# Optimization experiments

Hardware: AMD Instinct MI355X
Metric: run time of the kernel (lower is better)

## Reference

```python
import jax, jax.numpy as jnp
import numpy as np

LAMBDA_GEOMETRY = 1.0
EPS = 1e-4  # keep log() finite, mirroring valid (0,1) predictions


def setup_inputs() -> dict:
    key = jax.random.key(0)
    k1, k2, k3, k4 = jax.random.split(key, 4)
    m, H, W = 128, 128, 128
    Y_true_score = jax.random.uniform(k1, (m, 1, H, W), dtype=jnp.float32)
    Y_pred_score = jnp.clip(jax.random.uniform(k2, (m, 1, H, W), dtype=jnp.float32), EPS, 1.0 - EPS)
    Y_true_geometry = jax.random.uniform(k3, (m, 8, H, W), dtype=jnp.float32)
    Y_pred_geometry = jax.random.uniform(k4, (m, 8, H, W), dtype=jnp.float32)
    return {
        "Y_true_score": Y_true_score,
        "Y_pred_score": Y_pred_score,
        "Y_true_geometry": Y_true_geometry,
        "Y_pred_geometry": Y_pred_geometry,
    }


def reference(Y_true_score, Y_pred_score, Y_true_geometry, Y_pred_geometry):
    m = Y_true_score.shape[0]
    # --- weighted BCE score loss ---
    beta = 1.0 - jnp.sum(Y_true_score) / Y_true_score.size
    loss_pos = -beta * Y_true_score * jnp.log(Y_pred_score)
    loss_neg = -(1.0 - beta) * (1.0 - Y_true_score) * jnp.log(1.0 - Y_pred_score)
    loss_of_score = jnp.sum(loss_pos + loss_neg) / m
    # --- smoothed-L1 (Huber) geometry loss, vectorized over [m,8,H,W] ---
    l1 = jnp.abs(Y_true_geometry - Y_pred_geometry)
    huber = jnp.where(l1 < 1.0, 0.5 * l1 * l1, l1 - 0.5)
    n_c = Y_true_geometry.shape[1]  # 8
    n_pix = m * Y_true_geometry.shape[2] * Y_true_geometry.shape[3]
    loss_of_geometry = jnp.sum(huber) / n_c / n_pix * LAMBDA_GEOMETRY
    return loss_of_score + loss_of_geometry
```

## Files before the change

kernel.cpp:

```cpp
#include <hip/hip_runtime.h>


#define THREADS 256

__global__ __launch_bounds__(THREADS) void
loss_reduce(const float4* __restrict__ yts,
            const float4* __restrict__ yps,
            const float4* __restrict__ ytg,
            const float4* __restrict__ ypg,
            float4* __restrict__ partial,
            int n_s4, int n_g4) {
    const int tid = blockIdx.x * THREADS + threadIdx.x;
    const int T   = gridDim.x * THREADS;

    float s0 = 0.f, s1 = 0.f, s2 = 0.f, sg = 0.f;

    for (int i = tid; i < n_s4; i += T) {
        float4 t = yts[i];
        float4 p = yps[i];
        s0 += (t.x + t.y) + (t.z + t.w);
        s1 += t.x * __logf(p.x) + t.y * __logf(p.y)
            + t.z * __logf(p.z) + t.w * __logf(p.w);
        s2 += (1.f - t.x) * __logf(1.f - p.x) + (1.f - t.y) * __logf(1.f - p.y)
            + (1.f - t.z) * __logf(1.f - p.z) + (1.f - t.w) * __logf(1.f - p.w);
    }

    int i = tid;
    for (; i + 3 * T < n_g4; i += 4 * T) {
        float4 t0 = ytg[i];
        float4 t1 = ytg[i + T];
        float4 t2 = ytg[i + 2 * T];
        float4 t3 = ytg[i + 3 * T];
        float4 p0 = ypg[i];
        float4 p1 = ypg[i + T];
        float4 p2 = ypg[i + 2 * T];
        float4 p3 = ypg[i + 3 * T];

        #pragma unroll
        for (int k = 0; k < 4; ++k) {
            float4 t = (k == 0) ? t0 : (k == 1) ? t1 : (k == 2) ? t2 : t3;
            float4 p = (k == 0) ? p0 : (k == 1) ? p1 : (k == 2) ? p2 : p3;
            float dx = fabsf(t.x - p.x);
            float dy = fabsf(t.y - p.y);
            float dz = fabsf(t.z - p.z);
            float dw = fabsf(t.w - p.w);
            float hx = (dx < 1.f) ? 0.5f * dx * dx : dx - 0.5f;
            float hy = (dy < 1.f) ? 0.5f * dy * dy : dy - 0.5f;
            float hz = (dz < 1.f) ? 0.5f * dz * dz : dz - 0.5f;
            float hw = (dw < 1.f) ? 0.5f * dw * dw : dw - 0.5f;
            sg += (hx + hy) + (hz + hw);
        }
    }
    for (; i < n_g4; i += T) {
        float4 t = ytg[i];
        float4 p = ypg[i];
        float dx = fabsf(t.x - p.x);
        float dy = fabsf(t.y - p.y);
        float dz = fabsf(t.z - p.z);
        float dw = fabsf(t.w - p.w);
        float hx = (dx < 1.f) ? 0.5f * dx * dx : dx - 0.5f;
        float hy = (dy < 1.f) ? 0.5f * dy * dy : dy - 0.5f;
        float hz = (dz < 1.f) ? 0.5f * dz * dz : dz - 0.5f;
        float hw = (dw < 1.f) ? 0.5f * dw * dw : dw - 0.5f;
        sg += (hx + hy) + (hz + hw);
    }

    #pragma unroll
    for (int off = 32; off > 0; off >>= 1) {
        s0 += __shfl_down(s0, off);
        s1 += __shfl_down(s1, off);
        s2 += __shfl_down(s2, off);
        sg += __shfl_down(sg, off);
    }

    __shared__ float lds[4][4];
    const int wave = threadIdx.x >> 6;
    const int lane = threadIdx.x & 63;
    if (lane == 0) {
        lds[wave][0] = s0; lds[wave][1] = s1;
        lds[wave][2] = s2; lds[wave][3] = sg;
    }
    __syncthreads();
    if (threadIdx.x == 0) {
        float4 r;
        r.x = lds[0][0] + lds[1][0] + lds[2][0] + lds[3][0];
        r.y = lds[0][1] + lds[1][1] + lds[2][1] + lds[3][1];
        r.z = lds[0][2] + lds[1][2] + lds[2][2] + lds[3][2];
        r.w = lds[0][3] + lds[1][3] + lds[2][3] + lds[3][3];
        partial[blockIdx.x] = r;
    }
}

__global__ __launch_bounds__(THREADS) void
loss_finalize(const float4* __restrict__ partial, int nblocks,
              float* __restrict__ out,
              float inv_n_score, float inv_m, float inv_geo_div) {
    float s0 = 0.f, s1 = 0.f, s2 = 0.f, sg = 0.f;
    for (int i = threadIdx.x; i < nblocks; i += THREADS) {
        float4 v = partial[i];
        s0 += v.x; s1 += v.y; s2 += v.z; sg += v.w;
    }
    #pragma unroll
    for (int off = 32; off > 0; off >>= 1) {
        s0 += __shfl_down(s0, off);
        s1 += __shfl_down(s1, off);
        s2 += __shfl_down(s2, off);
        sg += __shfl_down(sg, off);
    }
    __shared__ float lds[4][4];
    const int wave = threadIdx.x >> 6;
    const int lane = threadIdx.x & 63;
    if (lane == 0) {
        lds[wave][0] = s0; lds[wave][1] = s1;
        lds[wave][2] = s2; lds[wave][3] = sg;
    }
    __syncthreads();
    if (threadIdx.x == 0) {
        const float S0 = lds[0][0] + lds[1][0] + lds[2][0] + lds[3][0];
        const float S1 = lds[0][1] + lds[1][1] + lds[2][1] + lds[3][1];
        const float S2 = lds[0][2] + lds[1][2] + lds[2][2] + lds[3][2];
        const float SG = lds[0][3] + lds[1][3] + lds[2][3] + lds[3][3];
        const float beta = 1.f - S0 * inv_n_score;
        const float loss_score = (-beta * S1 - (1.f - beta) * S2) * inv_m;
        const float loss_geo   = SG * inv_geo_div;
        out[0] = loss_score + loss_geo;
    }
}

extern "C" void kernel_launch(void* const* d_in, const int* in_sizes, int n_in,
                              void* d_out, int out_size, void* d_ws, size_t ws_size,
                              hipStream_t stream) {
    const float4* yts = (const float4*)d_in[0];
    const float4* yps = (const float4*)d_in[1];
    const float4* ytg = (const float4*)d_in[2];
    const float4* ypg = (const float4*)d_in[3];
    float* out = (float*)d_out;
    float4* partial = (float4*)d_ws;

    const int n_score = in_sizes[0];
    const int n_geo   = in_sizes[2];
    const int n_s4 = n_score / 4;
    const int n_g4 = n_geo / 4;

    int blocks = 2048;
    const size_t need = (size_t)blocks * sizeof(float4);
    if (ws_size < need) blocks = (int)(ws_size / sizeof(float4));

    const float inv_n_score = 1.f / (float)n_score;
    const float inv_m       = 1.f / 128.f;
    const float inv_geo_div = 1.f / (8.f * (float)n_score);

    loss_reduce<<<blocks, THREADS, 0, stream>>>(yts, yps, ytg, ypg, partial,
                                                n_s4, n_g4);
    loss_finalize<<<1, THREADS, 0, stream>>>(partial, blocks, out,
                                             inv_n_score, inv_m, inv_geo_div);
}
```

Baseline: 33.23 us.

## Fuse finalize into reduce kernel via last-block atomic counter; unroll geometry loop 8x

Merges the separate finalize launch into the main reduction kernel: each block publishes its partial, bumps an atomic counter, and the last block to arrive reduces all partials and writes the result. This removes the second kernel launch but adds a memset of the counter on the stream. The geometry loop is also unrolled to eight loads in flight per thread, and launch bounds gain a minimum-occupancy hint of 4, both aimed at more memory-level parallelism.

```diff
diff --git a/kernel.cpp b/kernel.cpp
--- a/kernel.cpp
+++ b/kernel.cpp
@@ -2,14 +2,30 @@
 
 
 #define THREADS 256
+#define MAXNB 2048
 
-__global__ __launch_bounds__(THREADS) void
-loss_reduce(const float4* __restrict__ yts,
-            const float4* __restrict__ yps,
-            const float4* __restrict__ ytg,
-            const float4* __restrict__ ypg,
-            float4* __restrict__ partial,
-            int n_s4, int n_g4) {
+__device__ __forceinline__ float huber4(float4 t, float4 p) {
+    float dx = fabsf(t.x - p.x);
+    float dy = fabsf(t.y - p.y);
+    float dz = fabsf(t.z - p.z);
+    float dw = fabsf(t.w - p.w);
+    float hx = (dx < 1.f) ? 0.5f * dx * dx : dx - 0.5f;
+    float hy = (dy < 1.f) ? 0.5f * dy * dy : dy - 0.5f;
+    float hz = (dz < 1.f) ? 0.5f * dz * dz : dz - 0.5f;
+    float hw = (dw < 1.f) ? 0.5f * dw * dw : dw - 0.5f;
+    return (hx + hy) + (hz + hw);
+}
+
+__global__ __launch_bounds__(THREADS, 4) void
+loss_fused(const float4* __restrict__ yts,
+           const float4* __restrict__ yps,
+           const float4* __restrict__ ytg,
+           const float4* __restrict__ ypg,
+           float4* __restrict__ partial,
+           unsigned* __restrict__ cnt,
+           float* __restrict__ out,
+           int n_s4, int n_g4,
+           float inv_n_score, float inv_m, float inv_geo_div) {
     const int tid = blockIdx.x * THREADS + threadIdx.x;
     const int T   = gridDim.x * THREADS;
 
@@ -26,43 +42,26 @@
     }
 
     int i = tid;
-    for (; i + 3 * T < n_g4; i += 4 * T) {
-        float4 t0 = ytg[i];
-        float4 t1 = ytg[i + T];
-        float4 t2 = ytg[i + 2 * T];
-        float4 t3 = ytg[i + 3 * T];
-        float4 p0 = ypg[i];
-        float4 p1 = ypg[i + T];
-        float4 p2 = ypg[i + 2 * T];
-        float4 p3 = ypg[i + 3 * T];
-
-        #pragma unroll
-        for (int k = 0; k < 4; ++k) {
-            float4 t = (k == 0) ? t0 : (k == 1) ? t1 : (k == 2) ? t2 : t3;
-            float4 p = (k == 0) ? p0 : (k == 1) ? p1 : (k == 2) ? p2 : p3;
-            float dx = fabsf(t.x - p.x);
-            float dy = fabsf(t.y - p.y);
-            float dz = fabsf(t.z - p.z);
-            float dw = fabsf(t.w - p.w);
-            float hx = (dx < 1.f) ? 0.5f * dx * dx : dx - 0.5f;
-            float hy = (dy < 1.f) ? 0.5f * dy * dy : dy - 0.5f;
-            float hz = (dz < 1.f) ? 0.5f * dz * dz : dz - 0.5f;
-            float hw = (dw < 1.f) ? 0.5f * dw * dw : dw - 0.5f;
-            sg += (hx + hy) + (hz + hw);
-        }
+    for (; i + 7 * T < n_g4; i += 8 * T) {
+        float4 t0 = ytg[i];         float4 p0 = ypg[i];
+        float4 t1 = ytg[i + T];     float4 p1 = ypg[i + T];
+        float4 t2 = ytg[i + 2 * T]; float4 p2 = ypg[i + 2 * T];
+        float4 t3 = ytg[i + 3 * T]; float4 p3 = ypg[i + 3 * T];
+        float4 t4 = ytg[i + 4 * T]; float4 p4 = ypg[i + 4 * T];
+        float4 t5 = ytg[i + 5 * T]; float4 p5 = ypg[i + 5 * T];
+        float4 t6 = ytg[i + 6 * T]; float4 p6 = ypg[i + 6 * T];
+        float4 t7 = ytg[i + 7 * T]; float4 p7 = ypg[i + 7 * T];
+        sg += huber4(t0, p0);
+        sg += huber4(t1, p1);
+        sg += huber4(t2, p2);
+        sg += huber4(t3, p3);
+        sg += huber4(t4, p4);
+        sg += huber4(t5, p5);
+        sg += huber4(t6, p6);
+        sg += huber4(t7, p7);
     }
     for (; i < n_g4; i += T) {
-        float4 t = ytg[i];
-        float4 p = ypg[i];
-        float dx = fabsf(t.x - p.x);
-        float dy = fabsf(t.y - p.y);
-        float dz = fabsf(t.z - p.z);
-        float dw = fabsf(t.w - p.w);
-        float hx = (dx < 1.f) ? 0.5f * dx * dx : dx - 0.5f;
-        float hy = (dy < 1.f) ? 0.5f * dy * dy : dy - 0.5f;
-        float hz = (dz < 1.f) ? 0.5f * dz * dz : dz - 0.5f;
-        float hw = (dw < 1.f) ? 0.5f * dw * dw : dw - 0.5f;
-        sg += (hx + hy) + (hz + hw);
+        sg += huber4(ytg[i], ypg[i]);
     }
 
     #pragma unroll
@@ -74,6 +73,7 @@
     }
 
     __shared__ float lds[4][4];
+    __shared__ int is_last;
     const int wave = threadIdx.x >> 6;
     const int lane = threadIdx.x & 63;
     if (lane == 0) {
@@ -88,42 +88,42 @@
         r.z = lds[0][2] + lds[1][2] + lds[2][2] + lds[3][2];
         r.w = lds[0][3] + lds[1][3] + lds[2][3] + lds[3][3];
         partial[blockIdx.x] = r;
-    }
-}
-
-__global__ __launch_bounds__(THREADS) void
-loss_finalize(const float4* __restrict__ partial, int nblocks,
-              float* __restrict__ out,
-              float inv_n_score, float inv_m, float inv_geo_div) {
-    float s0 = 0.f, s1 = 0.f, s2 = 0.f, sg = 0.f;
-    for (int i = threadIdx.x; i < nblocks; i += THREADS) {
-        float4 v = partial[i];
-        s0 += v.x; s1 += v.y; s2 += v.z; sg += v.w;
-    }
-    #pragma unroll
-    for (int off = 32; off > 0; off >>= 1) {
-        s0 += __shfl_down(s0, off);
-        s1 += __shfl_down(s1, off);
-        s2 += __shfl_down(s2, off);
-        sg += __shfl_down(sg, off);
-    }
-    __shared__ float lds[4][4];
-    const int wave = threadIdx.x >> 6;
-    const int lane = threadIdx.x & 63;
-    if (lane == 0) {
-        lds[wave][0] = s0; lds[wave][1] = s1;
-        lds[wave][2] = s2; lds[wave][3] = sg;
+        __threadfence();
+        unsigned old = atomicAdd(cnt, 1u);
+        is_last = (old == (unsigned)(gridDim.x - 1)) ? 1 : 0;
     }
     __syncthreads();
-    if (threadIdx.x == 0) {
-        const float S0 = lds[0][0] + lds[1][0] + lds[2][0] + lds[3][0];
-        const float S1 = lds[0][1] + lds[1][1] + lds[2][1] + lds[3][1];
-        const float S2 = lds[0][2] + lds[1][2] + lds[2][2] + lds[3][2];
-        const float SG = lds[0][3] + lds[1][3] + lds[2][3] + lds[3][3];
-        const float beta = 1.f - S0 * inv_n_score;
-        const float loss_score = (-beta * S1 - (1.f - beta) * S2) * inv_m;
-        const float loss_geo   = SG * inv_geo_div;
-        out[0] = loss_score + loss_geo;
+
+    if (is_last) {
+        __threadfence();
+        float a0 = 0.f, a1 = 0.f, a2 = 0.f, a3 = 0.f;
+        for (int j = threadIdx.x; j < (int)gridDim.x; j += THREADS) {
+            float4 v = partial[j];
+            a0 += v.x; a1 += v.y; a2 += v.z; a3 += v.w;
+        }
+        #pragma unroll
+        for (int off = 32; off > 0; off >>= 1) {
+            a0 += __shfl_down(a0, off);
+            a1 += __shfl_down(a1, off);
+            a2 += __shfl_down(a2, off);
+            a3 += __shfl_down(a3, off);
+        }
+        __syncthreads();
+        if (lane == 0) {
+            lds[wave][0] = a0; lds[wave][1] = a1;
+            lds[wave][2] = a2; lds[wave][3] = a3;
+        }
+        __syncthreads();
+        if (threadIdx.x == 0) {
+            const float S0 = lds[0][0] + lds[1][0] + lds[2][0] + lds[3][0];
+            const float S1 = lds[0][1] + lds[1][1] + lds[2][1] + lds[3][1];
+            const float S2 = lds[0][2] + lds[1][2] + lds[2][2] + lds[3][2];
+            const float SG = lds[0][3] + lds[1][3] + lds[2][3] + lds[3][3];
+            const float beta = 1.f - S0 * inv_n_score;
+            const float loss_score = (-beta * S1 - (1.f - beta) * S2) * inv_m;
+            const float loss_geo   = SG * inv_geo_div;
+            out[0] = loss_score + loss_geo;
+        }
     }
 }
 
@@ -135,23 +135,28 @@
     const float4* ytg = (const float4*)d_in[2];
     const float4* ypg = (const float4*)d_in[3];
     float* out = (float*)d_out;
-    float4* partial = (float4*)d_ws;
 
     const int n_score = in_sizes[0];
     const int n_geo   = in_sizes[2];
     const int n_s4 = n_score / 4;
     const int n_g4 = n_geo / 4;
 
-    int blocks = 2048;
-    const size_t need = (size_t)blocks * sizeof(float4);
-    if (ws_size < need) blocks = (int)(ws_size / sizeof(float4));
+    int blocks = MAXNB;
+    const size_t need = (size_t)blocks * sizeof(float4) + sizeof(unsigned);
+    if (ws_size < need)
+        blocks = (int)((ws_size - sizeof(unsigned)) / sizeof(float4));
+
+    float4* partial = (float4*)d_ws;
+    unsigned* cnt = (unsigned*)((char*)d_ws + (size_t)blocks * sizeof(float4));
 
     const float inv_n_score = 1.f / (float)n_score;
     const float inv_m       = 1.f / 128.f;
     const float inv_geo_div = 1.f / (8.f * (float)n_score);
 
-    loss_reduce<<<blocks, THREADS, 0, stream>>>(yts, yps, ytg, ypg, partial,
-                                                n_s4, n_g4);
-    loss_finalize<<<1, THREADS, 0, stream>>>(partial, blocks, out,
-                                             inv_n_score, inv_m, inv_geo_div);
+    hipMemsetAsync(cnt, 0, sizeof(unsigned), stream);
+
+    loss_fused<<<blocks, THREADS, 0, stream>>>(yts, yps, ytg, ypg,
+                                               partial, cnt, out,
+                                               n_s4, n_g4,
+                                               inv_n_score, inv_m, inv_geo_div);
 }
```

Result: slower. 100.8 us (+203.4%).

## Split reduction into dedicated geometry and score blocks with fixed per-thread work

Applied to the files above, without the earlier changes.

Adds a specialized kernel in which 4096 blocks each handle exactly four float4 pairs of geometry data and 512 blocks handle four float4 pairs of score data. Loops and bounds checks go away, and each thread issues all of its loads up front. It is meant to spread the memory traffic over more blocks and improve latency hiding compared with the grid-stride loop over 2048 blocks. The specialized path runs only when the input shape matches exactly; otherwise the original kernel is used, and the finalize step now reduces more partials.

```diff
diff --git a/kernel.cpp b/kernel.cpp
--- a/kernel.cpp
+++ b/kernel.cpp
@@ -2,6 +2,107 @@
 
 
 #define THREADS 256
+#define GEO_BLOCKS 4096
+#define SCORE_BLOCKS 512
+#define TOTAL_BLOCKS (GEO_BLOCKS + SCORE_BLOCKS)
+#define FALLBACK_BLOCKS 2048
+
+__device__ __forceinline__ float huber4f(float4 t, float4 p) {
+    float dx = fabsf(t.x - p.x);
+    float dy = fabsf(t.y - p.y);
+    float dz = fabsf(t.z - p.z);
+    float dw = fabsf(t.w - p.w);
+    float hx = (dx < 1.f) ? 0.5f * dx * dx : dx - 0.5f;
+    float hy = (dy < 1.f) ? 0.5f * dy * dy : dy - 0.5f;
+    float hz = (dz < 1.f) ? 0.5f * dz * dz : dz - 0.5f;
+    float hw = (dw < 1.f) ? 0.5f * dw * dw : dw - 0.5f;
+    return (hx + hy) + (hz + hw);
+}
+
+__device__ __forceinline__ void
+block_reduce_store(float s0, float s1, float s2, float sg,
+                   float4* __restrict__ partial) {
+    #pragma unroll
+    for (int off = 32; off > 0; off >>= 1) {
+        s0 += __shfl_down(s0, off);
+        s1 += __shfl_down(s1, off);
+        s2 += __shfl_down(s2, off);
+        sg += __shfl_down(sg, off);
+    }
+    __shared__ float lds[4][4];
+    const int wave = threadIdx.x >> 6;
+    const int lane = threadIdx.x & 63;
+    if (lane == 0) {
+        lds[wave][0] = s0; lds[wave][1] = s1;
+        lds[wave][2] = s2; lds[wave][3] = sg;
+    }
+    __syncthreads();
+    if (threadIdx.x == 0) {
+        float4 r;
+        r.x = lds[0][0] + lds[1][0] + lds[2][0] + lds[3][0];
+        r.y = lds[0][1] + lds[1][1] + lds[2][1] + lds[3][1];
+        r.z = lds[0][2] + lds[1][2] + lds[2][2] + lds[3][2];
+        r.w = lds[0][3] + lds[1][3] + lds[2][3] + lds[3][3];
+        partial[blockIdx.x] = r;
+    }
+}
+
+__global__ __launch_bounds__(THREADS) void
+loss_reduce_split(const float4* __restrict__ yts,
+                  const float4* __restrict__ yps,
+                  const float4* __restrict__ ytg,
+                  const float4* __restrict__ ypg,
+                  float4* __restrict__ partial) {
+    float s0 = 0.f, s1 = 0.f, s2 = 0.f, sg = 0.f;
+
+    if (blockIdx.x < GEO_BLOCKS) {
+        const int tid = blockIdx.x * THREADS + threadIdx.x;
+        const int Tg  = GEO_BLOCKS * THREADS;
+
+        float4 t0 = ytg[tid];
+        float4 t1 = ytg[tid + Tg];
+        float4 t2 = ytg[tid + 2 * Tg];
+        float4 t3 = ytg[tid + 3 * Tg];
+        float4 p0 = ypg[tid];
+        float4 p1 = ypg[tid + Tg];
+        float4 p2 = ypg[tid + 2 * Tg];
+        float4 p3 = ypg[tid + 3 * Tg];
+
+        #pragma unroll
+        for (int k = 0; k < 4; ++k) {
+            float4 t = (k == 0) ? t0 : (k == 1) ? t1 : (k == 2) ? t2 : t3;
+            float4 p = (k == 0) ? p0 : (k == 1) ? p1 : (k == 2) ? p2 : p3;
+            sg += huber4f(t, p);
+        }
+    } else {
+        const int tid = (blockIdx.x - GEO_BLOCKS) * THREADS + threadIdx.x;
+        const int Ts  = SCORE_BLOCKS * THREADS;
+
+        float4 a0 = yts[tid];
+        float4 a1 = yts[tid + Ts];
+        float4 a2 = yts[tid + 2 * Ts];
+        float4 a3 = yts[tid + 3 * Ts];
+        float4 b0 = yps[tid];
+        float4 b1 = yps[tid + Ts];
+        float4 b2 = yps[tid + 2 * Ts];
+        float4 b3 = yps[tid + 3 * Ts];
+
+        #pragma unroll
+        for (int k = 0; k < 4; ++k) {
+            float4 t = (k == 0) ? a0 : (k == 1) ? a1 : (k == 2) ? a2 : a3;
+            float4 p = (k == 0) ? b0 : (k == 1) ? b1 : (k == 2) ? b2 : b3;
+            s0 += (t.x + t.y) + (t.z + t.w);
+            s1 += t.x * __logf(p.x) + t.y * __logf(p.y)
+                + t.z * __logf(p.z) + t.w * __logf(p.w);
+            s2 += (1.f - t.x) * __logf(1.f - p.x)
+                + (1.f - t.y) * __logf(1.f - p.y)
+                + (1.f - t.z) * __logf(1.f - p.z)
+                + (1.f - t.w) * __logf(1.f - p.w);
+        }
+    }
+
+    block_reduce_store(s0, s1, s2, sg, partial);
+}
 
 __global__ __launch_bounds__(THREADS) void
 loss_reduce(const float4* __restrict__ yts,
@@ -35,60 +136,18 @@
         float4 p1 = ypg[i + T];
         float4 p2 = ypg[i + 2 * T];
         float4 p3 = ypg[i + 3 * T];
-
         #pragma unroll
         for (int k = 0; k < 4; ++k) {
             float4 t = (k == 0) ? t0 : (k == 1) ? t1 : (k == 2) ? t2 : t3;
             float4 p = (k == 0) ? p0 : (k == 1) ? p1 : (k == 2) ? p2 : p3;
-            float dx = fabsf(t.x - p.x);
-            float dy = fabsf(t.y - p.y);
-            float dz = fabsf(t.z - p.z);
-            float dw = fabsf(t.w - p.w);
-            float hx = (dx < 1.f) ? 0.5f * dx * dx : dx - 0.5f;
-            float hy = (dy < 1.f) ? 0.5f * dy * dy : dy - 0.5f;
-            float hz = (dz < 1.f) ? 0.5f * dz * dz : dz - 0.5f;
-            float hw = (dw < 1.f) ? 0.5f * dw * dw : dw - 0.5f;
-            sg += (hx + hy) + (hz + hw);
+            sg += huber4f(t, p);
         }
     }
     for (; i < n_g4; i += T) {
-        float4 t = ytg[i];
-        float4 p = ypg[i];
-        float dx = fabsf(t.x - p.x);
-        float dy = fabsf(t.y - p.y);
-        float dz = fabsf(t.z - p.z);
-        float dw = fabsf(t.w - p.w);
-        float hx = (dx < 1.f) ? 0.5f * dx * dx : dx - 0.5f;
-        float hy = (dy < 1.f) ? 0.5f * dy * dy : dy - 0.5f;
-        float hz = (dz < 1.f) ? 0.5f * dz * dz : dz - 0.5f;
-        float hw = (dw < 1.f) ? 0.5f * dw * dw : dw - 0.5f;
-        sg += (hx + hy) + (hz + hw);
-    }
-
-    #pragma unroll
-    for (int off = 32; off > 0; off >>= 1) {
-        s0 += __shfl_down(s0, off);
-        s1 += __shfl_down(s1, off);
-        s2 += __shfl_down(s2, off);
-        sg += __shfl_down(sg, off);
-    }
-
-    __shared__ float lds[4][4];
-    const int wave = threadIdx.x >> 6;
-    const int lane = threadIdx.x & 63;
-    if (lane == 0) {
-        lds[wave][0] = s0; lds[wave][1] = s1;
-        lds[wave][2] = s2; lds[wave][3] = sg;
-    }
-    __syncthreads();
-    if (threadIdx.x == 0) {
-        float4 r;
-        r.x = lds[0][0] + lds[1][0] + lds[2][0] + lds[3][0];
-        r.y = lds[0][1] + lds[1][1] + lds[2][1] + lds[3][1];
-        r.z = lds[0][2] + lds[1][2] + lds[2][2] + lds[3][2];
-        r.w = lds[0][3] + lds[1][3] + lds[2][3] + lds[3][3];
-        partial[blockIdx.x] = r;
-    }
+        sg += huber4f(ytg[i], ypg[i]);
+    }
+
+    block_reduce_store(s0, s1, s2, sg, partial);
 }
 
 __global__ __launch_bounds__(THREADS) void
@@ -142,16 +201,29 @@
     const int n_s4 = n_score / 4;
     const int n_g4 = n_geo / 4;
 
-    int blocks = 2048;
-    const size_t need = (size_t)blocks * sizeof(float4);
-    if (ws_size < need) blocks = (int)(ws_size / sizeof(float4));
-
     const float inv_n_score = 1.f / (float)n_score;
     const float inv_m       = 1.f / 128.f;
     const float inv_geo_div = 1.f / (8.f * (float)n_score);
 
-    loss_reduce<<<blocks, THREADS, 0, stream>>>(yts, yps, ytg, ypg, partial,
-                                                n_s4, n_g4);
-    loss_finalize<<<1, THREADS, 0, stream>>>(partial, blocks, out,
-                                             inv_n_score, inv_m, inv_geo_div);
-}
+    const bool shape_ok =
+        (n_g4 == 4 * GEO_BLOCKS * THREADS) &&
+        (n_s4 == 4 * SCORE_BLOCKS * THREADS);
+    const bool ws_ok = ws_size >= (size_t)TOTAL_BLOCKS * sizeof(float4);
+
+    if (shape_ok && ws_ok) {
+        loss_reduce_split<<<TOTAL_BLOCKS, THREADS, 0, stream>>>(
+            yts, yps, ytg, ypg, partial);
+        loss_finalize<<<1, THREADS, 0, stream>>>(partial, TOTAL_BLOCKS, out,
+                                                 inv_n_score, inv_m,
+                                                 inv_geo_div);
+    } else {
+        int blocks = FALLBACK_BLOCKS;
+        const size_t need = (size_t)blocks * sizeof(float4);
+        if (ws_size < need) blocks = (int)(ws_size / sizeof(float4));
+        loss_reduce<<<blocks, THREADS, 0, stream>>>(yts, yps, ytg, ypg,
+                                                    partial, n_s4, n_g4);
+        loss_finalize<<<1, THREADS, 0, stream>>>(partial, blocks, out,
+                                                 inv_n_score, inv_m,
+                                                 inv_geo_div);
+    }
+}
```

Result: slower. 35.91 us (+8.1%).
